# Kernel tuning notes

Measured on AMD Instinct MI355X. Metric: run time of the kernel, lower is better.

The kernel has to match this reference:

```python
import jax, jax.numpy as jnp
import numpy as np

B, N, DIM, H = 8, 1024, 1024, 16
D = DIM // H  # head dim = 64
SCALE = DIM ** (-0.5)  # NOTE: original uses full dim, not head dim


def setup_inputs() -> dict:
    key = jax.random.key(0)
    ks = jax.random.split(key, 8)
    x = jax.random.normal(ks[0], (B, N, DIM), dtype=jnp.float32)
    pos = jax.random.normal(ks[1], (B, N, DIM), dtype=jnp.float32)
    mask = jax.random.bernoulli(ks[2], 0.9, (B, N - 1))  # bool, [b, n-1]
    w_std = 0.02
    W_qk = jax.random.normal(ks[3], (2 * DIM, DIM), dtype=jnp.float32) * w_std  # Linear(dim, 2*dim_qk)
    W_v = jax.random.normal(ks[4], (DIM, DIM), dtype=jnp.float32) * w_std
    W_out = jax.random.normal(ks[5], (DIM, DIM), dtype=jnp.float32) * w_std
    b_out = jax.random.normal(ks[6], (DIM,), dtype=jnp.float32) * w_std
    return {"x": x, "mask": mask, "pos": pos, "W_qk": W_qk, "W_v": W_v,
            "W_out": W_out, "b_out": b_out}


def _split_heads(t):
    # b n (h d) -> b h n d
    b, n, _ = t.shape
    return t.reshape(b, n, H, D).transpose(0, 2, 1, 3)


def reference(x, mask, pos, W_qk, W_v, W_out, b_out):
    qk = x @ W_qk.T                       # [b, n, 2*dim]
    q, k = jnp.split(qk, 2, axis=-1)
    v = x @ W_v.T                         # [b, n, dim]
    q, k, v = _split_heads(q), _split_heads(k), _split_heads(v)  # [b,h,n,d]
    hpos = _split_heads(pos)
    q = q + hpos
    k = k + hpos
    dots = jnp.einsum('bhid,bhjd->bhij', q, k) * SCALE  # [b,h,n,n]
    mask_value = -jnp.finfo(dots.dtype).max
    # pad mask with True at position 0 (CLS token always visible)
    m = jnp.pad(mask, ((0, 0), (1, 0)), constant_values=True)  # [b, n]
    m2 = m[:, None, :] & m[:, :, None]                          # [b, n, n]
    dots = jnp.where(m2[:, None, :, :], dots, mask_value)
    attn = jax.nn.softmax(dots, axis=-1)
    out = jnp.einsum('bhij,bhjd->bhid', attn, v)  # [b,h,n,d]
    out = out.transpose(0, 2, 1, 3).reshape(x.shape[0], x.shape[1], DIM)  # b n (h d)
    out = out @ W_out.T + b_out  # dropout p=0.0 -> identity
    return out
```

## Files before the change

kernel.cpp:

```cpp
#include <hip/hip_runtime.h>


typedef unsigned short u16;
typedef short bf16x8 __attribute__((ext_vector_type(8)));
typedef float f32x4 __attribute__((ext_vector_type(4)));
typedef float f32x16 __attribute__((ext_vector_type(16)));

#define MFMA16(a, b, c) __builtin_amdgcn_mfma_f32_16x16x32_bf16((a), (b), (c), 0, 0, 0)
#define MFMA32(a, b, c) __builtin_amdgcn_mfma_f32_32x32x16_bf16((a), (b), (c), 0, 0, 0)

__device__ __forceinline__ u16 f2bf(float f) {
    union { float f; unsigned u; } x; x.f = f;
    unsigned r = x.u + 0x7fffu + ((x.u >> 16) & 1u);
    return (u16)(r >> 16);
}

__device__ __forceinline__ void gld16(const u16* g, u16* l) {
    __builtin_amdgcn_global_load_lds(
        (const __attribute__((address_space(1))) void*)g,
        (__attribute__((address_space(3))) void*)l, 16, 0, 0);
}

__global__ __launch_bounds__(256) void cast_all(
    const float* __restrict__ x, const float* __restrict__ wqk,
    const float* __restrict__ wv, const float* __restrict__ wout,
    u16* __restrict__ xbf, u16* __restrict__ wqkvbf, u16* __restrict__ woutbf) {
    int i = blockIdx.x * 256 + threadIdx.x;
    const float* src; u16* dst; int off;
    if (i < 2097152)      { src = x;    dst = xbf;              off = i; }
    else if (i < 2621440) { src = wqk;  dst = wqkvbf;           off = i - 2097152; }
    else if (i < 2883584) { src = wv;   dst = wqkvbf + 2097152; off = i - 2621440; }
    else                  { src = wout; dst = woutbf;           off = i - 2883584; }
    float4 v = ((const float4*)src)[off];
    ushort4 o;
    o.x = f2bf(v.x); o.y = f2bf(v.y); o.z = f2bf(v.z); o.w = f2bf(v.w);
    ((ushort4*)dst)[off] = o;
}

__global__ __launch_bounds__(256) void gemm_qk(
    const u16* __restrict__ A,
    const u16* __restrict__ Bw,
    const float* __restrict__ pos,
    u16* __restrict__ Q, u16* __restrict__ Kx) {
    const int n0 = blockIdx.x * 128, m0 = blockIdx.y * 128;
    const int t = threadIdx.x, w = t >> 6, ln = t & 63;
    const int l15 = ln & 15, l4 = ln >> 4;
    const int wm = (w >> 1) * 64, wn = (w & 1) * 64;

    __shared__ u16 As[128 * 64];
    __shared__ u16 Bs[128 * 64];

    f32x4 acc[4][4];
#pragma unroll
    for (int i = 0; i < 4; ++i)
#pragma unroll
        for (int j = 0; j < 4; ++j) acc[i][j] = (f32x4){0.f, 0.f, 0.f, 0.f};

    const int sr = ln >> 3;
    const int scx = ((ln & 7) ^ sr) * 8;
    const int x0 = (l15 & 7);
    for (int k0 = 0; k0 < 1024; k0 += 64) {
        __syncthreads();
#pragma unroll
        for (int p = 0; p < 4; ++p) {
            int rbase = w * 32 + p * 8;
            gld16(A  + (size_t)(m0 + rbase + sr) * 1024 + k0 + scx, &As[rbase * 64]);
            gld16(Bw + (size_t)(n0 + rbase + sr) * 1024 + k0 + scx, &Bs[rbase * 64]);
        }
        __syncthreads();
#pragma unroll
        for (int kt = 0; kt < 2; ++kt) {
            bf16x8 a[4], bfr[4];
#pragma unroll
            for (int mt = 0; mt < 4; ++mt)
                a[mt] = *(const bf16x8*)&As[(wm + mt * 16 + l15) * 64 + ((kt * 4 + l4) ^ x0) * 8];
#pragma unroll
            for (int nt = 0; nt < 4; ++nt)
                bfr[nt] = *(const bf16x8*)&Bs[(wn + nt * 16 + l15) * 64 + ((kt * 4 + l4) ^ x0) * 8];
#pragma unroll
            for (int mt = 0; mt < 4; ++mt)
#pragma unroll
                for (int nt = 0; nt < 4; ++nt)
                    acc[mt][nt] = MFMA16(a[mt], bfr[nt], acc[mt][nt]);
        }
    }
#pragma unroll
    for (int mt = 0; mt < 4; ++mt)
#pragma unroll
        for (int nt = 0; nt < 4; ++nt)
#pragma unroll
            for (int r = 0; r < 4; ++r) {
                int i = m0 + wm + mt * 16 + l4 * 4 + r;
                int j = n0 + wn + nt * 16 + l15;
                int bb = i >> 10, n = i & 1023;
                int jj = j & 1023;
                float v = acc[mt][nt][r] + pos[(size_t)i * 1024 + jj];
                int hh = jj >> 6, dd = jj & 63;
                size_t idx = (((size_t)(bb * 16 + hh)) * 1024 + n) * 64 + dd;
                if (j < 1024) Q[idx] = f2bf(v * 0.045084220027780106f);
                else          Kx[idx] = f2bf(v);
            }
}

__global__ __launch_bounds__(256) void gemm_v(
    const u16* __restrict__ Wv,
    const u16* __restrict__ X,
    u16* __restrict__ Vt) {
    const int n0 = blockIdx.x * 128, m0 = blockIdx.y * 128;
    const int bIdx = blockIdx.z;
    const u16* Xb = X + (size_t)bIdx * 1048576;
    const int t = threadIdx.x, w = t >> 6, ln = t & 63;
    const int l15 = ln & 15, l4 = ln >> 4;
    const int wm = (w >> 1) * 64, wn = (w & 1) * 64;

    __shared__ u16 As[128 * 64];
    __shared__ u16 Bs[128 * 64];

    f32x4 acc[4][4];
#pragma unroll
    for (int i = 0; i < 4; ++i)
#pragma unroll
        for (int j = 0; j < 4; ++j) acc[i][j] = (f32x4){0.f, 0.f, 0.f, 0.f};

    const int sr = ln >> 3;
    const int scx = ((ln & 7) ^ sr) * 8;
    const int x0 = (l15 & 7);
    for (int k0 = 0; k0 < 1024; k0 += 64) {
        __syncthreads();
#pragma unroll
        for (int p = 0; p < 4; ++p) {
            int rbase = w * 32 + p * 8;
            gld16(Wv + (size_t)(m0 + rbase + sr) * 1024 + k0 + scx, &As[rbase * 64]);
            gld16(Xb + (size_t)(n0 + rbase + sr) * 1024 + k0 + scx, &Bs[rbase * 64]);
        }
        __syncthreads();
#pragma unroll
        for (int kt = 0; kt < 2; ++kt) {
            bf16x8 a[4], bfr[4];
#pragma unroll
            for (int mt = 0; mt < 4; ++mt)
                a[mt] = *(const bf16x8*)&As[(wm + mt * 16 + l15) * 64 + ((kt * 4 + l4) ^ x0) * 8];
#pragma unroll
            for (int nt = 0; nt < 4; ++nt)
                bfr[nt] = *(const bf16x8*)&Bs[(wn + nt * 16 + l15) * 64 + ((kt * 4 + l4) ^ x0) * 8];
#pragma unroll
            for (int mt = 0; mt < 4; ++mt)
#pragma unroll
                for (int nt = 0; nt < 4; ++nt)
                    acc[mt][nt] = MFMA16(a[mt], bfr[nt], acc[mt][nt]);
        }
    }
#pragma unroll
    for (int mt = 0; mt < 4; ++mt)
#pragma unroll
        for (int nt = 0; nt < 4; ++nt)
#pragma unroll
            for (int r = 0; r < 4; ++r) {
                int i = m0 + wm + mt * 16 + l4 * 4 + r;
                int j = n0 + wn + nt * 16 + l15;
                Vt[((size_t)(bIdx * 1024 + i)) * 1024 + j] = f2bf(acc[mt][nt][r]);
            }
}

__global__ __launch_bounds__(64) void vsum_kernel(const u16* __restrict__ Vt,
                                                  float* __restrict__ Vsum) {
    int row = blockIdx.x, ln = threadIdx.x;
    const u16* p = Vt + (size_t)row * 1024 + ln * 16;
    uint4 a = *(const uint4*)p;
    uint4 bq = *(const uint4*)(p + 8);
    float s = 0.f;
    unsigned vv[8] = {a.x, a.y, a.z, a.w, bq.x, bq.y, bq.z, bq.w};
#pragma unroll
    for (int i = 0; i < 8; ++i) {
        s += __uint_as_float(vv[i] << 16);
        s += __uint_as_float(vv[i] & 0xffff0000u);
    }
#pragma unroll
    for (int d = 1; d < 64; d <<= 1) s += __shfl_xor(s, d);
    if (ln == 0) Vsum[row] = s;
}

__global__ __launch_bounds__(512) void attn_kernel(
    const u16* __restrict__ Q,
    const u16* __restrict__ Kx,
    const u16* __restrict__ Vt,
    const int* __restrict__ maskIn,
    const float* __restrict__ Vsum,
    u16* __restrict__ O) {
    const int gid = blockIdx.x;
    const int bh = gid & 127;
    const int qt = gid >> 7;
    const int b = bh >> 4, h = bh & 15;
    const int t = threadIdx.x, w = t >> 6, ln = t & 63;
    const int half = w >> 2, wq = w & 3;
    const int l31 = ln & 31, l5 = ln >> 5;

    __shared__ __align__(16) char lds[40960];
    u16* Ks = (u16*)(lds + half * 18432);
    u16* Vs = (u16*)(lds + half * 18432 + 9216);
    float* mch = (float*)(lds + 36864);

    for (int i = t; i < 1024; i += 512)
        mch[i] = (i == 0 || maskIn[b * 1023 + i - 1] != 0) ? 0.f : -1e30f;

    const size_t qkbase = (size_t)bh * 65536;
    const int q0 = qt * 128 + wq * 32;
    const int q = q0 + l31;

    bf16x8 bq[4];
#pragma unroll
    for (int kt = 0; kt < 4; ++kt)
        bq[kt] = *(const bf16x8*)(Q + qkbase + (size_t)q * 64 + kt * 16 + l5 * 8);

    float lsum = 0.f;
    f32x16 o0 = {0,0,0,0,0,0,0,0,0,0,0,0,0,0,0,0};
    f32x16 o1 = {0,0,0,0,0,0,0,0,0,0,0,0,0,0,0,0};

    const int th = t & 255;
    const int srow = th >> 2, sc = (th & 3) * 16;
    const int jbase = half * 512;

    for (int jt = 0; jt < 8; ++jt) {
        const int j0 = jbase + jt * 64;
        __syncthreads();
        {
            uint4 kv  = *(const uint4*)(Kx + qkbase + (size_t)(j0 + srow) * 64 + sc);
            uint4 kv2 = *(const uint4*)(Kx + qkbase + (size_t)(j0 + srow) * 64 + sc + 8);
            *(uint4*)&Ks[srow * 72 + sc] = kv;
            *(uint4*)&Ks[srow * 72 + sc + 8] = kv2;
            uint4 vv  = *(const uint4*)(Vt + qkbase + (size_t)srow * 1024 + j0 + sc);
            uint4 vv2 = *(const uint4*)(Vt + qkbase + (size_t)srow * 1024 + j0 + sc + 8);
            *(uint4*)&Vs[srow * 72 + sc] = vv;
            *(uint4*)&Vs[srow * 72 + sc + 8] = vv2;
        }
        __syncthreads();

        f32x16 st0 = {0,0,0,0,0,0,0,0,0,0,0,0,0,0,0,0};
        f32x16 st1 = {0,0,0,0,0,0,0,0,0,0,0,0,0,0,0,0};
#pragma unroll
        for (int ktk = 0; ktk < 4; ++ktk) {
            bf16x8 ak0 = *(const bf16x8*)&Ks[(l31) * 72 + ktk * 16 + l5 * 8];
            bf16x8 ak1 = *(const bf16x8*)&Ks[(32 + l31) * 72 + ktk * 16 + l5 * 8];
            st0 = MFMA32(ak0, bq[ktk], st0);
            st1 = MFMA32(ak1, bq[ktk], st1);
        }
#pragma unroll
        for (int g = 0; g < 4; ++g) {
            f32x4 cv0 = *(const f32x4*)&mch[j0 + g * 8 + l5 * 4];
            f32x4 cv1 = *(const f32x4*)&mch[j0 + 32 + g * 8 + l5 * 4];
#pragma unroll
            for (int r = 0; r < 4; ++r) {
                float p0 = __builtin_amdgcn_exp2f(st0[g * 4 + r] + cv0[r]);
                float p1 = __builtin_amdgcn_exp2f(st1[g * 4 + r] + cv1[r]);
                st0[g * 4 + r] = p0;
                st1[g * 4 + r] = p1;
                lsum += p0 + p1;
            }
        }
        unsigned pk0[8], pk1[8];
#pragma unroll
        for (int g = 0; g < 4; ++g) {
#pragma unroll
            for (int qq = 0; qq < 2; ++qq) {
                unsigned a0 = __float_as_uint(st0[g * 4 + 2 * qq]) + 0x8000u;
                unsigned a1 = __float_as_uint(st0[g * 4 + 2 * qq + 1]) + 0x8000u;
                pk0[2 * g + qq] = (a1 & 0xffff0000u) | (a0 >> 16);
                unsigned c0 = __float_as_uint(st1[g * 4 + 2 * qq]) + 0x8000u;
                unsigned c1 = __float_as_uint(st1[g * 4 + 2 * qq + 1]) + 0x8000u;
                pk1[2 * g + qq] = (c1 & 0xffff0000u) | (c0 >> 16);
            }
        }
        bf16x8 pf[4];
#pragma unroll
        for (int kt = 0; kt < 4; ++kt) {
            const int hh = kt & 1;
            unsigned own0, own1, off0, off1;
            if (kt < 2) {
                own0 = l5 ? pk0[4 * hh + 2] : pk0[4 * hh];
                own1 = l5 ? pk0[4 * hh + 3] : pk0[4 * hh + 1];
                off0 = l5 ? pk0[4 * hh]     : pk0[4 * hh + 2];
                off1 = l5 ? pk0[4 * hh + 1] : pk0[4 * hh + 3];
            } else {
                own0 = l5 ? pk1[4 * hh + 2] : pk1[4 * hh];
                own1 = l5 ? pk1[4 * hh + 3] : pk1[4 * hh + 1];
                off0 = l5 ? pk1[4 * hh]     : pk1[4 * hh + 2];
                off1 = l5 ? pk1[4 * hh + 1] : pk1[4 * hh + 3];
            }
            unsigned ex0 = (unsigned)__shfl_xor((int)off0, 32);
            unsigned ex1 = (unsigned)__shfl_xor((int)off1, 32);
            unsigned dw0 = l5 ? ex0 : own0;
            unsigned dw1 = l5 ? ex1 : own1;
            unsigned dw2 = l5 ? own0 : ex0;
            unsigned dw3 = l5 ? own1 : ex1;
            union { unsigned u[4]; bf16x8 v; } cv;
            cv.u[0] = dw0; cv.u[1] = dw1; cv.u[2] = dw2; cv.u[3] = dw3;
            pf[kt] = cv.v;
        }
#pragma unroll
        for (int kt = 0; kt < 4; ++kt) {
            bf16x8 av0 = *(const bf16x8*)&Vs[(l31) * 72 + kt * 16 + l5 * 8];
            bf16x8 av1 = *(const bf16x8*)&Vs[(32 + l31) * 72 + kt * 16 + l5 * 8];
            o0 = MFMA32(av0, pf[kt], o0);
            o1 = MFMA32(av1, pf[kt], o1);
        }
    }
    __syncthreads();
    float* comb = (float*)lds;
    if (half == 1) {
        float* dst = comb + ((size_t)(wq * 64 + ln)) * 33;
#pragma unroll
        for (int i = 0; i < 16; ++i) { dst[i] = o0[i]; dst[16 + i] = o1[i]; }
        dst[32] = lsum;
    }
    __syncthreads();
    if (half == 0) {
        const float* src = comb + ((size_t)(wq * 64 + ln)) * 33;
#pragma unroll
        for (int i = 0; i < 16; ++i) { o0[i] += src[i]; o1[i] += src[16 + i]; }
        lsum += src[32];
        float lrow = lsum + __shfl_xor(lsum, 32);
        const float linv = 1.f / lrow;
        const bool rqv = (mch[q] == 0.f);
        const int n = q0 + l31;
        u16* orow = O + ((size_t)(b * 1024 + n)) * 1024 + h * 64;
#pragma unroll
        for (int reg = 0; reg < 16; ++reg) {
            int d0 = (reg & 3) + 8 * (reg >> 2) + 4 * l5;
            float v0 = rqv ? o0[reg] * linv : Vsum[bh * 64 + d0] * 0.0009765625f;
            float v1 = rqv ? o1[reg] * linv : Vsum[bh * 64 + 32 + d0] * 0.0009765625f;
            orow[d0] = f2bf(v0);
            orow[32 + d0] = f2bf(v1);
        }
    }
}

__global__ __launch_bounds__(256) void gemm_out(
    const u16* __restrict__ A,
    const u16* __restrict__ Bw,
    const float* __restrict__ bias,
    float* __restrict__ out) {
    const int n0 = blockIdx.x * 128, m0 = blockIdx.y * 128;
    const int t = threadIdx.x, w = t >> 6, ln = t & 63;
    const int l15 = ln & 15, l4 = ln >> 4;
    const int wm = (w >> 1) * 64, wn = (w & 1) * 64;

    __shared__ u16 As[128 * 64];
    __shared__ u16 Bs[128 * 64];

    f32x4 acc[4][4];
#pragma unroll
    for (int i = 0; i < 4; ++i)
#pragma unroll
        for (int j = 0; j < 4; ++j) acc[i][j] = (f32x4){0.f, 0.f, 0.f, 0.f};

    const int sr = ln >> 3;
    const int scx = ((ln & 7) ^ sr) * 8;
    const int x0 = (l15 & 7);
    for (int k0 = 0; k0 < 1024; k0 += 64) {
        __syncthreads();
#pragma unroll
        for (int p = 0; p < 4; ++p) {
            int rbase = w * 32 + p * 8;
            gld16(A  + (size_t)(m0 + rbase + sr) * 1024 + k0 + scx, &As[rbase * 64]);
            gld16(Bw + (size_t)(n0 + rbase + sr) * 1024 + k0 + scx, &Bs[rbase * 64]);
        }
        __syncthreads();
#pragma unroll
        for (int kt = 0; kt < 2; ++kt) {
            bf16x8 a[4], bfr[4];
#pragma unroll
            for (int mt = 0; mt < 4; ++mt)
                a[mt] = *(const bf16x8*)&As[(wm + mt * 16 + l15) * 64 + ((kt * 4 + l4) ^ x0) * 8];
#pragma unroll
            for (int nt = 0; nt < 4; ++nt)
                bfr[nt] = *(const bf16x8*)&Bs[(wn + nt * 16 + l15) * 64 + ((kt * 4 + l4) ^ x0) * 8];
#pragma unroll
            for (int mt = 0; mt < 4; ++mt)
#pragma unroll
                for (int nt = 0; nt < 4; ++nt)
                    acc[mt][nt] = MFMA16(a[mt], bfr[nt], acc[mt][nt]);
        }
    }
#pragma unroll
    for (int mt = 0; mt < 4; ++mt)
#pragma unroll
        for (int nt = 0; nt < 4; ++nt)
#pragma unroll
            for (int r = 0; r < 4; ++r) {
                int i = m0 + wm + mt * 16 + l4 * 4 + r;
                int j = n0 + wn + nt * 16 + l15;
                out[(size_t)i * 1024 + j] = acc[mt][nt][r] + bias[j];
            }
}

extern "C" void kernel_launch(void* const* d_in, const int* in_sizes, int n_in,
                              void* d_out, int out_size, void* d_ws, size_t ws_size,
                              hipStream_t stream) {
    const float* x    = (const float*)d_in[0];
    const int*   mask = (const int*)d_in[1];
    const float* pos  = (const float*)d_in[2];
    const float* wqk  = (const float*)d_in[3];
    const float* wv   = (const float*)d_in[4];
    const float* wout = (const float*)d_in[5];
    const float* bout = (const float*)d_in[6];

    char* ws = (char*)d_ws;
    u16* xbf    = (u16*)(ws + 0);
    u16* wqkvbf = (u16*)(ws + 16777216);
    u16* woutbf = (u16*)(ws + 23068672);
    u16* Qb     = (u16*)(ws + 25165824);
    u16* Kb     = (u16*)(ws + 41943040);
    u16* Vtb    = (u16*)(ws + 58720256);
    float* Vsum = (float*)(ws + 16777216);

    cast_all<<<12288, 256, 0, stream>>>(x, wqk, wv, wout, xbf, wqkvbf, woutbf);

    gemm_qk<<<dim3(16, 64), 256, 0, stream>>>(xbf, wqkvbf, pos, Qb, Kb);
    gemm_v<<<dim3(8, 8, 8), 256, 0, stream>>>(wqkvbf + 2097152, xbf, Vtb);
    vsum_kernel<<<8192, 64, 0, stream>>>(Vtb, Vsum);
    attn_kernel<<<1024, 512, 0, stream>>>(Qb, Kb, Vtb, mask, Vsum, xbf);
    gemm_out<<<dim3(8, 64), 256, 0, stream>>>(xbf, woutbf, bout, (float*)d_out);
}
```

Baseline: 305.7 us.

## Load K/V MFMA fragments directly from global memory instead of LDS staging

Drops the per-tile cooperative copy of K and V into LDS and the two barriers around it. Each wave now loads its MFMA operand fragments straight from global memory into registers, with the V loads issued early so they overlap the softmax work. s_setprio is raised around the MFMA blocks. Each of the four waves in a half now fetches the same K/V data separately, so it relies on L1/L2 hits and adds register pressure, while removing LDS traffic and synchronisation stalls.

```diff
diff --git a/kernel.cpp b/kernel.cpp
--- a/kernel.cpp
+++ b/kernel.cpp
@@ -195,13 +195,13 @@
     const int half = w >> 2, wq = w & 3;
     const int l31 = ln & 31, l5 = ln >> 5;
 
-    __shared__ __align__(16) char lds[40960];
-    u16* Ks = (u16*)(lds + half * 18432);
-    u16* Vs = (u16*)(lds + half * 18432 + 9216);
-    float* mch = (float*)(lds + 36864);
+    __shared__ __align__(16) char lds[37888];
+    float* comb = (float*)lds;
+    float* mch = (float*)(lds + 33792);
 
     for (int i = t; i < 1024; i += 512)
         mch[i] = (i == 0 || maskIn[b * 1023 + i - 1] != 0) ? 0.f : -1e30f;
+    __syncthreads();
 
     const size_t qkbase = (size_t)bh * 65536;
     const int q0 = qt * 128 + wq * 32;
@@ -216,34 +216,41 @@
     f32x16 o0 = {0,0,0,0,0,0,0,0,0,0,0,0,0,0,0,0};
     f32x16 o1 = {0,0,0,0,0,0,0,0,0,0,0,0,0,0,0,0};
 
-    const int th = t & 255;
-    const int srow = th >> 2, sc = (th & 3) * 16;
     const int jbase = half * 512;
+    const int kfr0 = l31 * 64 + l5 * 8;
+    const int kfr1 = (32 + l31) * 64 + l5 * 8;
+    const int vfr0 = l31 * 1024 + l5 * 8;
+    const int vfr1 = (32 + l31) * 1024 + l5 * 8;
 
     for (int jt = 0; jt < 8; ++jt) {
         const int j0 = jbase + jt * 64;
-        __syncthreads();
-        {
-            uint4 kv  = *(const uint4*)(Kx + qkbase + (size_t)(j0 + srow) * 64 + sc);
-            uint4 kv2 = *(const uint4*)(Kx + qkbase + (size_t)(j0 + srow) * 64 + sc + 8);
-            *(uint4*)&Ks[srow * 72 + sc] = kv;
-            *(uint4*)&Ks[srow * 72 + sc + 8] = kv2;
-            uint4 vv  = *(const uint4*)(Vt + qkbase + (size_t)srow * 1024 + j0 + sc);
-            uint4 vv2 = *(const uint4*)(Vt + qkbase + (size_t)srow * 1024 + j0 + sc + 8);
-            *(uint4*)&Vs[srow * 72 + sc] = vv;
-            *(uint4*)&Vs[srow * 72 + sc + 8] = vv2;
-        }
-        __syncthreads();
+        const u16* Kp = Kx + qkbase + (size_t)j0 * 64;
+        const u16* Vp = Vt + qkbase + j0;
+
+        bf16x8 ak0[4], ak1[4];
+#pragma unroll
+        for (int ktk = 0; ktk < 4; ++ktk) {
+            ak0[ktk] = *(const bf16x8*)(Kp + kfr0 + ktk * 16);
+            ak1[ktk] = *(const bf16x8*)(Kp + kfr1 + ktk * 16);
+        }
 
         f32x16 st0 = {0,0,0,0,0,0,0,0,0,0,0,0,0,0,0,0};
         f32x16 st1 = {0,0,0,0,0,0,0,0,0,0,0,0,0,0,0,0};
+        __builtin_amdgcn_s_setprio(1);
 #pragma unroll
         for (int ktk = 0; ktk < 4; ++ktk) {
-            bf16x8 ak0 = *(const bf16x8*)&Ks[(l31) * 72 + ktk * 16 + l5 * 8];
-            bf16x8 ak1 = *(const bf16x8*)&Ks[(32 + l31) * 72 + ktk * 16 + l5 * 8];
-            st0 = MFMA32(ak0, bq[ktk], st0);
-            st1 = MFMA32(ak1, bq[ktk], st1);
-        }
+            st0 = MFMA32(ak0[ktk], bq[ktk], st0);
+            st1 = MFMA32(ak1[ktk], bq[ktk], st1);
+        }
+        __builtin_amdgcn_s_setprio(0);
+
+        bf16x8 av0[4], av1[4];
+#pragma unroll
+        for (int kt = 0; kt < 4; ++kt) {
+            av0[kt] = *(const bf16x8*)(Vp + vfr0 + kt * 16);
+            av1[kt] = *(const bf16x8*)(Vp + vfr1 + kt * 16);
+        }
+
 #pragma unroll
         for (int g = 0; g < 4; ++g) {
             f32x4 cv0 = *(const f32x4*)&mch[j0 + g * 8 + l5 * 4];
@@ -296,16 +303,14 @@
             cv.u[0] = dw0; cv.u[1] = dw1; cv.u[2] = dw2; cv.u[3] = dw3;
             pf[kt] = cv.v;
         }
+        __builtin_amdgcn_s_setprio(1);
 #pragma unroll
         for (int kt = 0; kt < 4; ++kt) {
-            bf16x8 av0 = *(const bf16x8*)&Vs[(l31) * 72 + kt * 16 + l5 * 8];
-            bf16x8 av1 = *(const bf16x8*)&Vs[(32 + l31) * 72 + kt * 16 + l5 * 8];
-            o0 = MFMA32(av0, pf[kt], o0);
-            o1 = MFMA32(av1, pf[kt], o1);
-        }
-    }
-    __syncthreads();
-    float* comb = (float*)lds;
+            o0 = MFMA32(av0[kt], pf[kt], o0);
+            o1 = MFMA32(av1[kt], pf[kt], o1);
+        }
+        __builtin_amdgcn_s_setprio(0);
+    }
     if (half == 1) {
         float* dst = comb + ((size_t)(wq * 64 + ln)) * 33;
 #pragma unroll
```

After: 371.0 us. 21.3% more time.
